# Kernel tuning notes

Hardware: AMD Instinct MI355X
Metric: run time of the kernel (lower is better)

The kernel has to match this reference:

```python
import jax, jax.numpy as jnp
import numpy as np


def _mlp(x, W1, b1, W2, b2, W3, b3):
    # flatten -> fc(784,512) -> relu -> fc(512,128) -> relu -> fc(128,C)
    h = x.reshape(x.shape[0], -1)
    h = jax.nn.relu(h @ W1.T + b1)
    h = jax.nn.relu(h @ W2.T + b2)
    return h @ W3.T + b3


def setup_inputs() -> dict:
    key = jax.random.key(0)
    ks = jax.random.split(key, 6)
    B, Bu, C, D = 65536, 4096, 10, 28 * 28
    return {
        "x": jax.random.uniform(ks[0], (B, 28, 28), jnp.float32),
        "y": jax.random.randint(ks[1], (B,), 0, C),
        "x_unlab": jax.random.uniform(ks[2], (Bu, 28, 28), jnp.float32),
        "W1": jax.random.normal(ks[3], (512, D), jnp.float32) * 0.03,
        "b1": jnp.zeros((512,), jnp.float32),
        "W2": jax.random.normal(ks[4], (128, 512), jnp.float32) * 0.05,
        "b2": jnp.zeros((128,), jnp.float32),
        "W3": jax.random.normal(ks[5], (C, 128), jnp.float32) * 0.08,
        "b3": jnp.zeros((C,), jnp.float32),
    }


def reference(x, y, x_unlab, W1, b1, W2, b2, W3, b3):
    n_classes = W3.shape[0]
    # ---- labeled branch: BCEWithLogitsLoss(mean) vs one-hot targets ----
    logits = _mlp(x, W1, b1, W2, b2, W3, b3)  # [B, C]
    t = jax.nn.one_hot(y, n_classes, dtype=logits.dtype)
    bce = jnp.mean(jnp.maximum(logits, 0.0) - logits * t
                   + jnp.log1p(jnp.exp(-jnp.abs(logits))))
    # ---- unlabeled branch: semantic loss ----
    # sem_loss(probs): s[c] = sum_i p_i[c] * prod_{j != i} (1 - p_j[c]);
    # return mean over classes of -log(s). Done in log domain with a single
    # O(Bu) leave-one-out sum instead of the original O(Bu^2) double loop.
    o_u = _mlp(x_unlab, W1, b1, W2, b2, W3, b3)       # [Bu, C]
    logp = jax.nn.log_sigmoid(o_u)                     # log p
    log1mp = jax.nn.log_sigmoid(-o_u)                  # log (1 - p)
    loo = jnp.sum(log1mp, axis=0, keepdims=True) - log1mp  # leave-one-out log-prod
    log_s = jax.scipy.special.logsumexp(logp + loo, axis=0)  # [C]
    sl = jnp.mean(-log_s)
    # compute_loss returns (bce, sl); stacked here as a length-2 vector
    return jnp.stack([bce, sl])
```

## Files before the change

### kernel.cpp

```cpp
#include <hip/hip_runtime.h>
#include <hip/hip_bf16.h>
#include <stdint.h>

typedef unsigned short ushort_t;
typedef __bf16 bf16x8 __attribute__((ext_vector_type(8)));
typedef float f32x4 __attribute__((ext_vector_type(4)));

__device__ __forceinline__ ushort_t f2bf(float f) {
    union { float f; unsigned u; } v; v.f = f;
    unsigned u = v.u;
    unsigned r = u + 0x7fffu + ((u >> 16) & 1u);
    return (ushort_t)(r >> 16);
}
__device__ __forceinline__ float bf2f(ushort_t h) {
    union { unsigned u; float f; } v; v.u = ((unsigned)h) << 16;
    return v.f;
}

#define GLDS16(gsrc, ldst)                                                    \
    __builtin_amdgcn_global_load_lds(                                         \
        (const __attribute__((address_space(1))) void*)(gsrc),                \
        (__attribute__((address_space(3))) void*)(ldst), 16, 0, 0)

__global__ __launch_bounds__(256) void prep_kernel(
    const float* __restrict__ W1, const float* __restrict__ W2,
    ushort_t* __restrict__ W1p, ushort_t* __restrict__ W2b,
    float* __restrict__ stats)
{
    int idx = blockIdx.x * 256 + threadIdx.x;
    if (idx < 512 * 800) {
        int n = idx / 800, k = idx - n * 800;
        W1p[idx] = (k < 784) ? f2bf(W1[n * 784 + k]) : (ushort_t)0;
    }
    if (idx < 128 * 512) W2b[idx] = f2bf(W2[idx]);
    if (idx == 0) stats[0] = 0.0f;
}

__global__ __launch_bounds__(256) void gemm1f_kernel(
    const float* __restrict__ x, const float* __restrict__ xu,
    const ushort_t* __restrict__ W1p, const float* __restrict__ b1,
    ushort_t* __restrict__ h1)
{
    __shared__ ushort_t As[2][128 * 32];
    __shared__ ushort_t Bs[2][128 * 32];

    const int b = blockIdx.x;
    const int xcd = b & 7, s = b >> 3;
    const int tile_n = s & 3;
    const int tile_m = xcd * 68 + (s >> 2);

    const int tid = threadIdx.x;
    const int w = tid >> 6, lane = tid & 63;
    const int wm = w >> 1, wn = w & 1;
    const int quad = lane >> 4, lc = lane & 15;
    const int row_in = lane >> 2;
    const int koff = (lane & 3) * 8;

    const int arow = tid >> 1;
    const int akoff = (tid & 1) * 16;
    const int grow = tile_m * 128 + arow;
    const float* asrc = (grow < 65536) ? (x + (size_t)grow * 784)
                                       : (xu + (size_t)(grow - 65536) * 784);
    ushort_t* adst0 = &As[0][arow * 32 + akoff];
    ushort_t* adst1 = &As[1][arow * 32 + akoff];

    f32x4 acc[4][4];
#pragma unroll
    for (int i = 0; i < 4; i++)
#pragma unroll
        for (int j = 0; j < 4; j++)
#pragma unroll
            for (int r = 0; r < 4; r++) acc[i][j][r] = 0.0f;

    float4 p0a, p0b, p0c, p0d, p1a, p1b, p1c, p1d;
    {
        const float4* q0 = (const float4*)(asrc + akoff);
        p0a = q0[0]; p0b = q0[1]; p0c = q0[2]; p0d = q0[3];
        const float4* q1 = (const float4*)(asrc + 32 + akoff);
        p1a = q1[0]; p1b = q1[1]; p1c = q1[2]; p1d = q1[3];
    }

    for (int k0 = 0; k0 < 800; k0 += 64) {
        const bool has2 = (k0 + 32) < 800;

#pragma unroll
        for (int c = 0; c < 2; c++) {
            int row = (w * 2 + c) * 16 + row_in;
            const ushort_t* srcB =
                W1p + (size_t)(tile_n * 128 + row) * 800 + k0 + koff;
            GLDS16(srcB, &Bs[0][(w * 2 + c) * 512]);
        }
        if (has2) {
#pragma unroll
            for (int c = 0; c < 2; c++) {
                int row = (w * 2 + c) * 16 + row_in;
                const ushort_t* srcB =
                    W1p + (size_t)(tile_n * 128 + row) * 800 + k0 + 32 + koff;
                GLDS16(srcB, &Bs[1][(w * 2 + c) * 512]);
            }
        }

        {
            uint4 lo, hi;
            if (k0 + akoff <= 768) {
                lo.x = ((unsigned)f2bf(p0a.y) << 16) | f2bf(p0a.x);
                lo.y = ((unsigned)f2bf(p0a.w) << 16) | f2bf(p0a.z);
                lo.z = ((unsigned)f2bf(p0b.y) << 16) | f2bf(p0b.x);
                lo.w = ((unsigned)f2bf(p0b.w) << 16) | f2bf(p0b.z);
                hi.x = ((unsigned)f2bf(p0c.y) << 16) | f2bf(p0c.x);
                hi.y = ((unsigned)f2bf(p0c.w) << 16) | f2bf(p0c.z);
                hi.z = ((unsigned)f2bf(p0d.y) << 16) | f2bf(p0d.x);
                hi.w = ((unsigned)f2bf(p0d.w) << 16) | f2bf(p0d.z);
            } else {
                lo = make_uint4(0, 0, 0, 0);
                hi = make_uint4(0, 0, 0, 0);
            }
            *(uint4*)adst0 = lo;
            *(uint4*)(adst0 + 8) = hi;
        }
        if (has2) {
            uint4 lo, hi;
            if (k0 + 32 + akoff <= 768) {
                lo.x = ((unsigned)f2bf(p1a.y) << 16) | f2bf(p1a.x);
                lo.y = ((unsigned)f2bf(p1a.w) << 16) | f2bf(p1a.z);
                lo.z = ((unsigned)f2bf(p1b.y) << 16) | f2bf(p1b.x);
                lo.w = ((unsigned)f2bf(p1b.w) << 16) | f2bf(p1b.z);
                hi.x = ((unsigned)f2bf(p1c.y) << 16) | f2bf(p1c.x);
                hi.y = ((unsigned)f2bf(p1c.w) << 16) | f2bf(p1c.z);
                hi.z = ((unsigned)f2bf(p1d.y) << 16) | f2bf(p1d.x);
                hi.w = ((unsigned)f2bf(p1d.w) << 16) | f2bf(p1d.z);
            } else {
                lo = make_uint4(0, 0, 0, 0);
                hi = make_uint4(0, 0, 0, 0);
            }
            *(uint4*)adst1 = lo;
            *(uint4*)(adst1 + 8) = hi;
        }

        {
            int kn0 = k0 + 64 + akoff;
            if (kn0 <= 768) {
                const float4* q = (const float4*)(asrc + kn0);
                p0a = q[0]; p0b = q[1]; p0c = q[2]; p0d = q[3];
            }
            int kn1 = k0 + 96 + akoff;
            if (kn1 <= 768) {
                const float4* q = (const float4*)(asrc + kn1);
                p1a = q[0]; p1b = q[1]; p1c = q[2]; p1d = q[3];
            }
        }
        __syncthreads();

        {
            bf16x8 af[4], bfr[4];
#pragma unroll
            for (int i = 0; i < 4; i++)
                af[i] = *(const bf16x8*)&As[0][(wm * 64 + i * 16 + lc) * 32 + quad * 8];
#pragma unroll
            for (int j = 0; j < 4; j++)
                bfr[j] = *(const bf16x8*)&Bs[0][(wn * 64 + j * 16 + lc) * 32 + quad * 8];
#pragma unroll
            for (int i = 0; i < 4; i++)
#pragma unroll
                for (int j = 0; j < 4; j++)
                    acc[i][j] = __builtin_amdgcn_mfma_f32_16x16x32_bf16(
                        af[i], bfr[j], acc[i][j], 0, 0, 0);
        }
        if (has2) {
            bf16x8 af[4], bfr[4];
#pragma unroll
            for (int i = 0; i < 4; i++)
                af[i] = *(const bf16x8*)&As[1][(wm * 64 + i * 16 + lc) * 32 + quad * 8];
#pragma unroll
            for (int j = 0; j < 4; j++)
                bfr[j] = *(const bf16x8*)&Bs[1][(wn * 64 + j * 16 + lc) * 32 + quad * 8];
#pragma unroll
            for (int i = 0; i < 4; i++)
#pragma unroll
                for (int j = 0; j < 4; j++)
                    acc[i][j] = __builtin_amdgcn_mfma_f32_16x16x32_bf16(
                        af[i], bfr[j], acc[i][j], 0, 0, 0);
        }
        __syncthreads();
    }

    float bias[4];
#pragma unroll
    for (int j = 0; j < 4; j++)
        bias[j] = b1[tile_n * 128 + wn * 64 + j * 16 + lc];
#pragma unroll
    for (int i = 0; i < 4; i++) {
        int gr0 = tile_m * 128 + wm * 64 + i * 16 + quad * 4;
#pragma unroll
        for (int j = 0; j < 4; j++) {
            int gc = tile_n * 128 + wn * 64 + j * 16 + lc;
#pragma unroll
            for (int r = 0; r < 4; r++) {
                float v = acc[i][j][r] + bias[j];
                v = fmaxf(v, 0.0f);
                h1[(size_t)(gr0 + r) * 512 + gc] = f2bf(v);
            }
        }
    }
}

__global__ __launch_bounds__(256) void gemm23_kernel(
    const ushort_t* __restrict__ h1, const ushort_t* __restrict__ W2b,
    const float* __restrict__ b2, const int* __restrict__ y,
    const float* __restrict__ W3, const float* __restrict__ b3,
    float* __restrict__ stats, float* __restrict__ logits_u)
{
    __shared__ ushort_t As[2][64 * 32];
    __shared__ ushort_t Bs[2][128 * 32];
    __shared__ float W3s[1280];
    __shared__ float b3s[10];
    __shared__ float red[4];

    const int tid = threadIdx.x;
    const int w = tid >> 6, lane = tid & 63;
    const int wm = w >> 1, wn = w & 1;
    const int quad = lane >> 4, lc = lane & 15;
    const int row_in = lane >> 2;
    const int koff = (lane & 3) * 8;
    const int tile_m = blockIdx.x;

    for (int i = tid; i < 1280; i += 256) W3s[i] = W3[i];
    if (tid < 10) b3s[tid] = b3[tid];

    f32x4 acc[2][4];
#pragma unroll
    for (int i = 0; i < 2; i++)
#pragma unroll
        for (int j = 0; j < 4; j++)
#pragma unroll
            for (int r = 0; r < 4; r++) acc[i][j][r] = 0.0f;

    for (int k0 = 0; k0 < 512; k0 += 64) {
#pragma unroll
        for (int p = 0; p < 2; p++) {
            {
                int rowA = w * 16 + row_in;
                const ushort_t* srcA =
                    h1 + (size_t)(tile_m * 64 + rowA) * 512 + k0 + p * 32 + koff;
                GLDS16(srcA, &As[p][w * 512]);
            }
#pragma unroll
            for (int c = 0; c < 2; c++) {
                int rowB = (w * 2 + c) * 16 + row_in;
                const ushort_t* srcB =
                    W2b + (size_t)rowB * 512 + k0 + p * 32 + koff;
                GLDS16(srcB, &Bs[p][(w * 2 + c) * 512]);
            }
        }
        __syncthreads();
#pragma unroll
        for (int p = 0; p < 2; p++) {
            bf16x8 af[2], bfr[4];
#pragma unroll
            for (int i = 0; i < 2; i++)
                af[i] = *(const bf16x8*)&As[p][(wm * 32 + i * 16 + lc) * 32 + quad * 8];
#pragma unroll
            for (int j = 0; j < 4; j++)
                bfr[j] = *(const bf16x8*)&Bs[p][(wn * 64 + j * 16 + lc) * 32 + quad * 8];
#pragma unroll
            for (int i = 0; i < 2; i++)
#pragma unroll
                for (int j = 0; j < 4; j++)
                    acc[i][j] = __builtin_amdgcn_mfma_f32_16x16x32_bf16(
                        af[i], bfr[j], acc[i][j], 0, 0, 0);
        }
        __syncthreads();
    }

    ushort_t* h2s = &Bs[0][0];
    float bias[4];
#pragma unroll
    for (int j = 0; j < 4; j++) bias[j] = b2[wn * 64 + j * 16 + lc];
#pragma unroll
    for (int i = 0; i < 2; i++) {
        int row0 = wm * 32 + i * 16 + quad * 4;
#pragma unroll
        for (int j = 0; j < 4; j++) {
            int col = wn * 64 + j * 16 + lc;
#pragma unroll
            for (int r = 0; r < 4; r++) {
                float v = fmaxf(acc[i][j][r] + bias[j], 0.0f);
                h2s[(row0 + r) * 128 + col] = f2bf(v);
            }
        }
    }
    __syncthreads();

    const size_t row0g = (size_t)tile_m * 64;
    float bce_part = 0.0f;
    for (int o = tid; o < 640; o += 256) {
        int r = o / 10, c = o - r * 10;
        size_t grw = row0g + r;
        float a = b3s[c];
        const ushort_t* hr = &h2s[r * 128];
        const float* wr = &W3s[c * 128];
#pragma unroll 8
        for (int k = 0; k < 128; k++) a += bf2f(hr[k]) * wr[k];
        if (grw < 65536) {
            float t = (y[grw] == c) ? 1.0f : 0.0f;
            bce_part += fmaxf(a, 0.0f) - a * t + log1pf(__expf(-fabsf(a)));
        } else {
            logits_u[(grw - 65536) * 10 + c] = a;
        }
    }
#pragma unroll
    for (int s = 32; s > 0; s >>= 1) bce_part += __shfl_down(bce_part, s, 64);
    if ((tid & 63) == 0) red[tid >> 6] = bce_part;
    __syncthreads();
    if (tid == 0) atomicAdd(stats, red[0] + red[1] + red[2] + red[3]);
}

__global__ __launch_bounds__(640) void finisher_kernel(
    const float* __restrict__ logits_u, const float* __restrict__ stats,
    float* __restrict__ out)
{
    __shared__ float Rs[64][10];
    __shared__ float Rm[64][10];
    __shared__ float Scol[10], Mcol[10];

    const int tid = threadIdx.x;
    const int g = tid / 10, c = tid - g * 10;
    float s = 0.0f, m = -1e30f;
    for (int i = g; i < 4096; i += 64) {
        float o = logits_u[i * 10 + c];
        s += fminf(-o, 0.0f) - log1pf(__expf(-fabsf(o)));
        m = fmaxf(m, o);
    }
    Rs[g][c] = s;
    Rm[g][c] = m;
    __syncthreads();
    if (tid < 10) {
        float ss = 0.0f, mm = -1e30f;
        for (int gg = 0; gg < 64; gg++) {
            ss += Rs[gg][tid];
            mm = fmaxf(mm, Rm[gg][tid]);
        }
        Scol[tid] = ss;
        Mcol[tid] = mm;
    }
    __syncthreads();
    float e = 0.0f;
    float mm = Mcol[c];
    for (int i = g; i < 4096; i += 64)
        e += __expf(logits_u[i * 10 + c] - mm);
    Rs[g][c] = e;
    __syncthreads();
    if (tid == 0) {
        float sl = 0.0f;
        for (int cc = 0; cc < 10; cc++) {
            float ee = 0.0f;
            for (int gg = 0; gg < 64; gg++) ee += Rs[gg][cc];
            sl += -(Scol[cc] + Mcol[cc] + __logf(ee));
        }
        sl *= 0.1f;
        out[0] = stats[0] * (1.0f / (65536.0f * 10.0f));
        out[1] = sl;
    }
}

extern "C" void kernel_launch(void* const* d_in, const int* in_sizes, int n_in,
                              void* d_out, int out_size, void* d_ws,
                              size_t ws_size, hipStream_t stream)
{
    const float* x  = (const float*)d_in[0];
    const int*   y  = (const int*)d_in[1];
    const float* xu = (const float*)d_in[2];
    const float* W1 = (const float*)d_in[3];
    const float* b1 = (const float*)d_in[4];
    const float* W2 = (const float*)d_in[5];
    const float* b2 = (const float*)d_in[6];
    const float* W3 = (const float*)d_in[7];
    const float* b3 = (const float*)d_in[8];
    float* out = (float*)d_out;

    char* ws = (char*)d_ws;
    ushort_t* W1p      = (ushort_t*)(ws + 0);
    ushort_t* W2b      = (ushort_t*)(ws + 819200);
    float*    stats    = (float*)(ws + 950272);
    float*    logits_u = (float*)(ws + 950528);
    ushort_t* h1       = (ushort_t*)(ws + 1114368);

    prep_kernel<<<1600, 256, 0, stream>>>(W1, W2, W1p, W2b, stats);
    gemm1f_kernel<<<2176, 256, 0, stream>>>(x, xu, W1p, b1, h1);
    gemm23_kernel<<<1088, 256, 0, stream>>>(h1, W2b, b2, y, W3, b3, stats,
                                            logits_u);
    finisher_kernel<<<1, 640, 0, stream>>>(logits_u, stats, out);
    (void)in_sizes; (void)n_in; (void)out_size; (void)ws_size;
}
```

Before: 503.3 us.

## Pre-convert inputs to bf16 and run LDS-free register-fed GEMM1

Adds a separate pass that converts x and x_unlab to a padded bf16 buffer in workspace, then a new GEMM1 kernel that loads MFMA operands straight from global memory into registers with software double-buffering, skipping LDS and __syncthreads. The goal is to remove in-loop fp32-to-bf16 conversion and LDS staging from the main GEMM. In exchange it adds an extra full read and write of the input (about 110 MB bf16 written, then re-read), and the direct global loads give no LDS reuse across waves. The new path only runs if the workspace is large enough, otherwise the old kernel is used.

Result: slower. 608.2 us (+20.8%).

```diff
diff --git a/kernel.cpp b/kernel.cpp
--- a/kernel.cpp
+++ b/kernel.cpp
@@ -34,6 +34,130 @@
     }
     if (idx < 128 * 512) W2b[idx] = f2bf(W2[idx]);
     if (idx == 0) stats[0] = 0.0f;
+}
+
+__global__ __launch_bounds__(256) void xconvert_kernel(
+    const float* __restrict__ x, const float* __restrict__ xu,
+    ushort_t* __restrict__ Xb)
+{
+    int idx = blockIdx.x * 256 + threadIdx.x;
+    int r = idx / 50, c = idx - r * 50;
+    uint4 lo, hi;
+    if (c < 49) {
+        const float* src = (r < 65536) ? (x + (size_t)r * 784)
+                                       : (xu + (size_t)(r - 65536) * 784);
+        const float4* p = (const float4*)(src + c * 16);
+        float4 f0 = p[0], f1 = p[1], f2 = p[2], f3 = p[3];
+        lo.x = ((unsigned)f2bf(f0.y) << 16) | f2bf(f0.x);
+        lo.y = ((unsigned)f2bf(f0.w) << 16) | f2bf(f0.z);
+        lo.z = ((unsigned)f2bf(f1.y) << 16) | f2bf(f1.x);
+        lo.w = ((unsigned)f2bf(f1.w) << 16) | f2bf(f1.z);
+        hi.x = ((unsigned)f2bf(f2.y) << 16) | f2bf(f2.x);
+        hi.y = ((unsigned)f2bf(f2.w) << 16) | f2bf(f2.z);
+        hi.z = ((unsigned)f2bf(f3.y) << 16) | f2bf(f3.x);
+        hi.w = ((unsigned)f2bf(f3.w) << 16) | f2bf(f3.z);
+    } else {
+        lo = make_uint4(0, 0, 0, 0);
+        hi = make_uint4(0, 0, 0, 0);
+    }
+    uint4* dst = (uint4*)(Xb + (size_t)r * 800 + c * 16);
+    dst[0] = lo;
+    dst[1] = hi;
+}
+
+__global__ __launch_bounds__(256) void gemm1reg_kernel(
+    const ushort_t* __restrict__ Xb, const ushort_t* __restrict__ W1p,
+    const float* __restrict__ b1, ushort_t* __restrict__ h1)
+{
+    const int b = blockIdx.x;
+    const int xcd = b & 7, s = b >> 3;
+    const int tile_n = s & 3;
+    const int tile_m = xcd * 68 + (s >> 2);
+
+    const int tid = threadIdx.x;
+    const int w = tid >> 6, lane = tid & 63;
+    const int wm = w >> 1, wn = w & 1;
+    const int quad = lane >> 4, lc = lane & 15;
+
+    const ushort_t* aptr[4];
+    const ushort_t* bptr[4];
+#pragma unroll
+    for (int i = 0; i < 4; i++) {
+        int row = tile_m * 128 + wm * 64 + i * 16 + lc;
+        aptr[i] = Xb + (size_t)row * 800 + quad * 8;
+    }
+#pragma unroll
+    for (int j = 0; j < 4; j++) {
+        int row = tile_n * 128 + wn * 64 + j * 16 + lc;
+        bptr[j] = W1p + (size_t)row * 800 + quad * 8;
+    }
+
+    f32x4 acc[4][4];
+#pragma unroll
+    for (int i = 0; i < 4; i++)
+#pragma unroll
+        for (int j = 0; j < 4; j++)
+#pragma unroll
+            for (int r = 0; r < 4; r++) acc[i][j][r] = 0.0f;
+
+    bf16x8 aA[4], bA[4], aB[4], bB[4];
+#pragma unroll
+    for (int i = 0; i < 4; i++) {
+        aA[i] = *(const bf16x8*)(aptr[i]);
+        bA[i] = *(const bf16x8*)(bptr[i]);
+    }
+
+    for (int k0 = 0; k0 < 800; k0 += 64) {
+        const bool hasB = (k0 + 32) < 800;
+        const bool hasN = (k0 + 64) < 800;
+        if (hasB) {
+#pragma unroll
+            for (int i = 0; i < 4; i++) {
+                aB[i] = *(const bf16x8*)(aptr[i] + k0 + 32);
+                bB[i] = *(const bf16x8*)(bptr[i] + k0 + 32);
+            }
+        }
+#pragma unroll
+        for (int i = 0; i < 4; i++)
+#pragma unroll
+            for (int j = 0; j < 4; j++)
+                acc[i][j] = __builtin_amdgcn_mfma_f32_16x16x32_bf16(
+                    aA[i], bA[j], acc[i][j], 0, 0, 0);
+        if (hasN) {
+#pragma unroll
+            for (int i = 0; i < 4; i++) {
+                aA[i] = *(const bf16x8*)(aptr[i] + k0 + 64);
+                bA[i] = *(const bf16x8*)(bptr[i] + k0 + 64);
+            }
+        }
+        if (hasB) {
+#pragma unroll
+            for (int i = 0; i < 4; i++)
+#pragma unroll
+                for (int j = 0; j < 4; j++)
+                    acc[i][j] = __builtin_amdgcn_mfma_f32_16x16x32_bf16(
+                        aB[i], bB[j], acc[i][j], 0, 0, 0);
+        }
+    }
+
+    float bias[4];
+#pragma unroll
+    for (int j = 0; j < 4; j++)
+        bias[j] = b1[tile_n * 128 + wn * 64 + j * 16 + lc];
+#pragma unroll
+    for (int i = 0; i < 4; i++) {
+        int gr0 = tile_m * 128 + wm * 64 + i * 16 + quad * 4;
+#pragma unroll
+        for (int j = 0; j < 4; j++) {
+            int gc = tile_n * 128 + wn * 64 + j * 16 + lc;
+#pragma unroll
+            for (int r = 0; r < 4; r++) {
+                float v = acc[i][j][r] + bias[j];
+                v = fmaxf(v, 0.0f);
+                h1[(size_t)(gr0 + r) * 512 + gc] = f2bf(v);
+            }
+        }
+    }
 }
 
 __global__ __launch_bounds__(256) void gemm1f_kernel(
@@ -82,7 +206,6 @@
 
     for (int k0 = 0; k0 < 800; k0 += 64) {
         const bool has2 = (k0 + 32) < 800;
-
 #pragma unroll
         for (int c = 0; c < 2; c++) {
             int row = (w * 2 + c) * 16 + row_in;
@@ -99,7 +222,6 @@
                 GLDS16(srcB, &Bs[1][(w * 2 + c) * 512]);
             }
         }
-
         {
             uint4 lo, hi;
             if (k0 + akoff <= 768) {
@@ -136,7 +258,6 @@
             *(uint4*)adst1 = lo;
             *(uint4*)(adst1 + 8) = hi;
         }
-
         {
             int kn0 = k0 + 64 + akoff;
             if (kn0 <= 768) {
@@ -150,7 +271,6 @@
             }
         }
         __syncthreads();
-
         {
             bf16x8 af[4], bfr[4];
 #pragma unroll
@@ -384,9 +504,16 @@
     float*    stats    = (float*)(ws + 950272);
     float*    logits_u = (float*)(ws + 950528);
     ushort_t* h1       = (ushort_t*)(ws + 1114368);
+    ushort_t* Xb       = (ushort_t*)(ws + 72417536);
+    const size_t FAST_WS_NEED = 183828736;
 
     prep_kernel<<<1600, 256, 0, stream>>>(W1, W2, W1p, W2b, stats);
-    gemm1f_kernel<<<2176, 256, 0, stream>>>(x, xu, W1p, b1, h1);
+    if (ws_size >= FAST_WS_NEED) {
+        xconvert_kernel<<<13600, 256, 0, stream>>>(x, xu, Xb);
+        gemm1reg_kernel<<<2176, 256, 0, stream>>>(Xb, W1p, b1, h1);
+    } else {
+        gemm1f_kernel<<<2176, 256, 0, stream>>>(x, xu, W1p, b1, h1);
+    }
     gemm23_kernel<<<1088, 256, 0, stream>>>(h1, W2b, b2, y, W3, b3, stats,
                                             logits_u);
     finisher_kernel<<<1, 640, 0, stream>>>(logits_u, stats, out);
```

## Fuse layer-1 and layer-2/3 GEMMs into one kernel keeping h1 in LDS

Applied to the files above, without the earlier changes.

Merges the first-layer GEMM and the second/third-layer kernel into a single kernel that processes 64-row tiles. Each tile loops over the four 128-column chunks of h1, stages each chunk in padded LDS, and accumulates it straight into the layer-2 result. This removes the global write and read of the large bf16 h1 intermediate and one kernel launch. In exchange, each block re-reads and re-converts its x rows four times and streams all of W1. The M tile also shrinks to 64 and W2 fragments are read directly from global memory, and the padded LDS stride adds a bank-conflict and alignment trade-off.

Result: slower. 576.3 us (+14.5%).

```diff
diff --git a/kernel.cpp b/kernel.cpp
--- a/kernel.cpp
+++ b/kernel.cpp
@@ -15,6 +15,9 @@
 __device__ __forceinline__ float bf2f(ushort_t h) {
     union { unsigned u; float f; } v; v.u = ((unsigned)h) << 16;
     return v.f;
+}
+__device__ __forceinline__ unsigned packbf(float a, float b) {
+    return ((unsigned)f2bf(b) << 16) | f2bf(a);
 }
 
 #define GLDS16(gsrc, ldst)                                                    \
@@ -36,18 +39,27 @@
     if (idx == 0) stats[0] = 0.0f;
 }
 
-__global__ __launch_bounds__(256) void gemm1f_kernel(
+#define AS_STRIDE 36
+#define H_STRIDE  136
+
+__global__ __launch_bounds__(256) void fused_kernel(
     const float* __restrict__ x, const float* __restrict__ xu,
-    const ushort_t* __restrict__ W1p, const float* __restrict__ b1,
-    ushort_t* __restrict__ h1)
+    const ushort_t* __restrict__ W1p, const ushort_t* __restrict__ W2b,
+    const float* __restrict__ b1, const float* __restrict__ b2,
+    const int* __restrict__ y, const float* __restrict__ W3,
+    const float* __restrict__ b3,
+    float* __restrict__ stats, float* __restrict__ logits_u)
 {
-    __shared__ ushort_t As[2][128 * 32];
-    __shared__ ushort_t Bs[2][128 * 32];
-
-    const int b = blockIdx.x;
-    const int xcd = b & 7, s = b >> 3;
-    const int tile_n = s & 3;
-    const int tile_m = xcd * 68 + (s >> 2);
+    __shared__ ushort_t smem[2 * 64 * AS_STRIDE + 2 * 128 * 32];
+    __shared__ float W3s[1280];
+    __shared__ float b3s[10];
+    __shared__ float red[4];
+
+    ushort_t* As0 = smem;
+    ushort_t* As1 = smem + 64 * AS_STRIDE;
+    ushort_t* Bs0 = smem + 2 * 64 * AS_STRIDE;
+    ushort_t* Bs1 = Bs0 + 128 * 32;
+    ushort_t* hs  = smem;
 
     const int tid = threadIdx.x;
     const int w = tid >> 6, lane = tid & 63;
@@ -55,249 +67,206 @@
     const int quad = lane >> 4, lc = lane & 15;
     const int row_in = lane >> 2;
     const int koff = (lane & 3) * 8;
-
-    const int arow = tid >> 1;
-    const int akoff = (tid & 1) * 16;
-    const int grow = tile_m * 128 + arow;
-    const float* asrc = (grow < 65536) ? (x + (size_t)grow * 784)
-                                       : (xu + (size_t)(grow - 65536) * 784);
-    ushort_t* adst0 = &As[0][arow * 32 + akoff];
-    ushort_t* adst1 = &As[1][arow * 32 + akoff];
-
-    f32x4 acc[4][4];
-#pragma unroll
-    for (int i = 0; i < 4; i++)
+    const int tile = blockIdx.x;
+    const size_t m0 = (size_t)tile * 64;
+
+    for (int i = tid; i < 1280; i += 256) W3s[i] = W3[i];
+    if (tid < 10) b3s[tid] = b3[tid];
+
+    const int arow = tid >> 2;
+    const int akoff = (tid & 3) * 8;
+    const size_t grow = m0 + arow;
+    const float* asrc = (grow < 65536) ? (x + grow * 784)
+                                       : (xu + (grow - 65536) * 784);
+    ushort_t* adst0 = &As0[arow * AS_STRIDE + akoff];
+    ushort_t* adst1 = &As1[arow * AS_STRIDE + akoff];
+
+    f32x4 h2acc[2][4];
+#pragma unroll
+    for (int i = 0; i < 2; i++)
 #pragma unroll
         for (int j = 0; j < 4; j++)
 #pragma unroll
-            for (int r = 0; r < 4; r++) acc[i][j][r] = 0.0f;
-
-    float4 p0a, p0b, p0c, p0d, p1a, p1b, p1c, p1d;
-    {
-        const float4* q0 = (const float4*)(asrc + akoff);
-        p0a = q0[0]; p0b = q0[1]; p0c = q0[2]; p0d = q0[3];
-        const float4* q1 = (const float4*)(asrc + 32 + akoff);
-        p1a = q1[0]; p1b = q1[1]; p1c = q1[2]; p1d = q1[3];
-    }
-
-    for (int k0 = 0; k0 < 800; k0 += 64) {
-        const bool has2 = (k0 + 32) < 800;
-
-#pragma unroll
-        for (int c = 0; c < 2; c++) {
-            int row = (w * 2 + c) * 16 + row_in;
-            const ushort_t* srcB =
-                W1p + (size_t)(tile_n * 128 + row) * 800 + k0 + koff;
-            GLDS16(srcB, &Bs[0][(w * 2 + c) * 512]);
-        }
-        if (has2) {
+            for (int r = 0; r < 4; r++) h2acc[i][j][r] = 0.0f;
+
+    for (int nc = 0; nc < 4; nc++) {
+        f32x4 acc[2][4];
+#pragma unroll
+        for (int i = 0; i < 2; i++)
+#pragma unroll
+            for (int j = 0; j < 4; j++)
+#pragma unroll
+                for (int r = 0; r < 4; r++) acc[i][j][r] = 0.0f;
+
+        float4 p0a, p0b, p1a, p1b;
+        {
+            const float4* q0 = (const float4*)(asrc + akoff);
+            p0a = q0[0]; p0b = q0[1];
+            const float4* q1 = (const float4*)(asrc + 32 + akoff);
+            p1a = q1[0]; p1b = q1[1];
+        }
+
+        for (int k0 = 0; k0 < 800; k0 += 64) {
+            const bool has2 = (k0 + 32) < 800;
 #pragma unroll
             for (int c = 0; c < 2; c++) {
                 int row = (w * 2 + c) * 16 + row_in;
                 const ushort_t* srcB =
-                    W1p + (size_t)(tile_n * 128 + row) * 800 + k0 + 32 + koff;
-                GLDS16(srcB, &Bs[1][(w * 2 + c) * 512]);
-            }
+                    W1p + (size_t)(nc * 128 + row) * 800 + k0 + koff;
+                GLDS16(srcB, &Bs0[(w * 2 + c) * 512]);
+            }
+            if (has2) {
+#pragma unroll
+                for (int c = 0; c < 2; c++) {
+                    int row = (w * 2 + c) * 16 + row_in;
+                    const ushort_t* srcB =
+                        W1p + (size_t)(nc * 128 + row) * 800 + k0 + 32 + koff;
+                    GLDS16(srcB, &Bs1[(w * 2 + c) * 512]);
+                }
+            }
+            {
+                uint4 u;
+                if (k0 + akoff <= 776) {
+                    u.x = packbf(p0a.x, p0a.y);
+                    u.y = packbf(p0a.z, p0a.w);
+                    u.z = packbf(p0b.x, p0b.y);
+                    u.w = packbf(p0b.z, p0b.w);
+                } else {
+                    u = make_uint4(0, 0, 0, 0);
+                }
+                *(uint4*)adst0 = u;
+            }
+            if (has2) {
+                uint4 u;
+                if (k0 + 32 + akoff <= 776) {
+                    u.x = packbf(p1a.x, p1a.y);
+                    u.y = packbf(p1a.z, p1a.w);
+                    u.z = packbf(p1b.x, p1b.y);
+                    u.w = packbf(p1b.z, p1b.w);
+                } else {
+                    u = make_uint4(0, 0, 0, 0);
+                }
+                *(uint4*)adst1 = u;
+            }
+            {
+                int kn0 = k0 + 64 + akoff;
+                if (kn0 <= 776) {
+                    const float4* q = (const float4*)(asrc + kn0);
+                    p0a = q[0]; p0b = q[1];
+                }
+                int kn1 = k0 + 96 + akoff;
+                if (kn1 <= 776) {
+                    const float4* q = (const float4*)(asrc + kn1);
+                    p1a = q[0]; p1b = q[1];
+                }
+            }
+            __syncthreads();
+            {
+                bf16x8 af[2], bfr[4];
+#pragma unroll
+                for (int i = 0; i < 2; i++)
+                    af[i] = *(const bf16x8*)
+                        &As0[(wm * 32 + i * 16 + lc) * AS_STRIDE + quad * 8];
+#pragma unroll
+                for (int j = 0; j < 4; j++)
+                    bfr[j] = *(const bf16x8*)
+                        &Bs0[(wn * 64 + j * 16 + lc) * 32 + quad * 8];
+#pragma unroll
+                for (int i = 0; i < 2; i++)
+#pragma unroll
+                    for (int j = 0; j < 4; j++)
+                        acc[i][j] = __builtin_amdgcn_mfma_f32_16x16x32_bf16(
+                            af[i], bfr[j], acc[i][j], 0, 0, 0);
+            }
+            if (has2) {
+                bf16x8 af[2], bfr[4];
+#pragma unroll
+                for (int i = 0; i < 2; i++)
+                    af[i] = *(const bf16x8*)
+                        &As1[(wm * 32 + i * 16 + lc) * AS_STRIDE + quad * 8];
+#pragma unroll
+                for (int j = 0; j < 4; j++)
+                    bfr[j] = *(const bf16x8*)
+                        &Bs1[(wn * 64 + j * 16 + lc) * 32 + quad * 8];
+#pragma unroll
+                for (int i = 0; i < 2; i++)
+#pragma unroll
+                    for (int j = 0; j < 4; j++)
+                        acc[i][j] = __builtin_amdgcn_mfma_f32_16x16x32_bf16(
+                            af[i], bfr[j], acc[i][j], 0, 0, 0);
+            }
+            __syncthreads();
         }
 
         {
-            uint4 lo, hi;
-            if (k0 + akoff <= 768) {
-                lo.x = ((unsigned)f2bf(p0a.y) << 16) | f2bf(p0a.x);
-                lo.y = ((unsigned)f2bf(p0a.w) << 16) | f2bf(p0a.z);
-                lo.z = ((unsigned)f2bf(p0b.y) << 16) | f2bf(p0b.x);
-                lo.w = ((unsigned)f2bf(p0b.w) << 16) | f2bf(p0b.z);
-                hi.x = ((unsigned)f2bf(p0c.y) << 16) | f2bf(p0c.x);
-                hi.y = ((unsigned)f2bf(p0c.w) << 16) | f2bf(p0c.z);
-                hi.z = ((unsigned)f2bf(p0d.y) << 16) | f2bf(p0d.x);
-                hi.w = ((unsigned)f2bf(p0d.w) << 16) | f2bf(p0d.z);
-            } else {
-                lo = make_uint4(0, 0, 0, 0);
-                hi = make_uint4(0, 0, 0, 0);
-            }
-            *(uint4*)adst0 = lo;
-            *(uint4*)(adst0 + 8) = hi;
-        }
-        if (has2) {
-            uint4 lo, hi;
-            if (k0 + 32 + akoff <= 768) {
-                lo.x = ((unsigned)f2bf(p1a.y) << 16) | f2bf(p1a.x);
-                lo.y = ((unsigned)f2bf(p1a.w) << 16) | f2bf(p1a.z);
-                lo.z = ((unsigned)f2bf(p1b.y) << 16) | f2bf(p1b.x);
-                lo.w = ((unsigned)f2bf(p1b.w) << 16) | f2bf(p1b.z);
-                hi.x = ((unsigned)f2bf(p1c.y) << 16) | f2bf(p1c.x);
-                hi.y = ((unsigned)f2bf(p1c.w) << 16) | f2bf(p1c.z);
-                hi.z = ((unsigned)f2bf(p1d.y) << 16) | f2bf(p1d.x);
-                hi.w = ((unsigned)f2bf(p1d.w) << 16) | f2bf(p1d.z);
-            } else {
-                lo = make_uint4(0, 0, 0, 0);
-                hi = make_uint4(0, 0, 0, 0);
-            }
-            *(uint4*)adst1 = lo;
-            *(uint4*)(adst1 + 8) = hi;
-        }
-
-        {
-            int kn0 = k0 + 64 + akoff;
-            if (kn0 <= 768) {
-                const float4* q = (const float4*)(asrc + kn0);
-                p0a = q[0]; p0b = q[1]; p0c = q[2]; p0d = q[3];
-            }
-            int kn1 = k0 + 96 + akoff;
-            if (kn1 <= 768) {
-                const float4* q = (const float4*)(asrc + kn1);
-                p1a = q[0]; p1b = q[1]; p1c = q[2]; p1d = q[3];
+            float bias[4];
+#pragma unroll
+            for (int j = 0; j < 4; j++)
+                bias[j] = b1[nc * 128 + wn * 64 + j * 16 + lc];
+#pragma unroll
+            for (int i = 0; i < 2; i++) {
+                int r0 = wm * 32 + i * 16 + quad * 4;
+#pragma unroll
+                for (int j = 0; j < 4; j++) {
+                    int col = wn * 64 + j * 16 + lc;
+#pragma unroll
+                    for (int r = 0; r < 4; r++) {
+                        float v = fmaxf(acc[i][j][r] + bias[j], 0.0f);
+                        hs[(r0 + r) * H_STRIDE + col] = f2bf(v);
+                    }
+                }
             }
         }
         __syncthreads();
 
-        {
-            bf16x8 af[4], bfr[4];
-#pragma unroll
-            for (int i = 0; i < 4; i++)
-                af[i] = *(const bf16x8*)&As[0][(wm * 64 + i * 16 + lc) * 32 + quad * 8];
+#pragma unroll
+        for (int p = 0; p < 4; p++) {
+            bf16x8 af[2], bfr[4];
+#pragma unroll
+            for (int i = 0; i < 2; i++)
+                af[i] = *(const bf16x8*)
+                    &hs[(wm * 32 + i * 16 + lc) * H_STRIDE + p * 32 + quad * 8];
 #pragma unroll
             for (int j = 0; j < 4; j++)
-                bfr[j] = *(const bf16x8*)&Bs[0][(wn * 64 + j * 16 + lc) * 32 + quad * 8];
-#pragma unroll
-            for (int i = 0; i < 4; i++)
+                bfr[j] = *(const bf16x8*)
+                    (W2b + (size_t)(wn * 64 + j * 16 + lc) * 512
+                         + nc * 128 + p * 32 + quad * 8);
+#pragma unroll
+            for (int i = 0; i < 2; i++)
 #pragma unroll
                 for (int j = 0; j < 4; j++)
-                    acc[i][j] = __builtin_amdgcn_mfma_f32_16x16x32_bf16(
-                        af[i], bfr[j], acc[i][j], 0, 0, 0);
-        }
-        if (has2) {
-            bf16x8 af[4], bfr[4];
-#pragma unroll
-            for (int i = 0; i < 4; i++)
-                af[i] = *(const bf16x8*)&As[1][(wm * 64 + i * 16 + lc) * 32 + quad * 8];
-#pragma unroll
-            for (int j = 0; j < 4; j++)
-                bfr[j] = *(const bf16x8*)&Bs[1][(wn * 64 + j * 16 + lc) * 32 + quad * 8];
-#pragma unroll
-            for (int i = 0; i < 4; i++)
-#pragma unroll
-                for (int j = 0; j < 4; j++)
-                    acc[i][j] = __builtin_amdgcn_mfma_f32_16x16x32_bf16(
-                        af[i], bfr[j], acc[i][j], 0, 0, 0);
+                    h2acc[i][j] = __builtin_amdgcn_mfma_f32_16x16x32_bf16(
+                        af[i], bfr[j], h2acc[i][j], 0, 0, 0);
         }
         __syncthreads();
     }
 
-    float bias[4];
-#pragma unroll
-    for (int j = 0; j < 4; j++)
-        bias[j] = b1[tile_n * 128 + wn * 64 + j * 16 + lc];
-#pragma unroll
-    for (int i = 0; i < 4; i++) {
-        int gr0 = tile_m * 128 + wm * 64 + i * 16 + quad * 4;
-#pragma unroll
-        for (int j = 0; j < 4; j++) {
-            int gc = tile_n * 128 + wn * 64 + j * 16 + lc;
-#pragma unroll
-            for (int r = 0; r < 4; r++) {
-                float v = acc[i][j][r] + bias[j];
-                v = fmaxf(v, 0.0f);
-                h1[(size_t)(gr0 + r) * 512 + gc] = f2bf(v);
-            }
-        }
-    }
-}
-
-__global__ __launch_bounds__(256) void gemm23_kernel(
-    const ushort_t* __restrict__ h1, const ushort_t* __restrict__ W2b,
-    const float* __restrict__ b2, const int* __restrict__ y,
-    const float* __restrict__ W3, const float* __restrict__ b3,
-    float* __restrict__ stats, float* __restrict__ logits_u)
-{
-    __shared__ ushort_t As[2][64 * 32];
-    __shared__ ushort_t Bs[2][128 * 32];
-    __shared__ float W3s[1280];
-    __shared__ float b3s[10];
-    __shared__ float red[4];
-
-    const int tid = threadIdx.x;
-    const int w = tid >> 6, lane = tid & 63;
-    const int wm = w >> 1, wn = w & 1;
-    const int quad = lane >> 4, lc = lane & 15;
-    const int row_in = lane >> 2;
-    const int koff = (lane & 3) * 8;
-    const int tile_m = blockIdx.x;
-
-    for (int i = tid; i < 1280; i += 256) W3s[i] = W3[i];
-    if (tid < 10) b3s[tid] = b3[tid];
-
-    f32x4 acc[2][4];
-#pragma unroll
-    for (int i = 0; i < 2; i++)
-#pragma unroll
-        for (int j = 0; j < 4; j++)
-#pragma unroll
-            for (int r = 0; r < 4; r++) acc[i][j][r] = 0.0f;
-
-    for (int k0 = 0; k0 < 512; k0 += 64) {
-#pragma unroll
-        for (int p = 0; p < 2; p++) {
-            {
-                int rowA = w * 16 + row_in;
-                const ushort_t* srcA =
-                    h1 + (size_t)(tile_m * 64 + rowA) * 512 + k0 + p * 32 + koff;
-                GLDS16(srcA, &As[p][w * 512]);
-            }
-#pragma unroll
-            for (int c = 0; c < 2; c++) {
-                int rowB = (w * 2 + c) * 16 + row_in;
-                const ushort_t* srcB =
-                    W2b + (size_t)rowB * 512 + k0 + p * 32 + koff;
-                GLDS16(srcB, &Bs[p][(w * 2 + c) * 512]);
-            }
-        }
-        __syncthreads();
-#pragma unroll
-        for (int p = 0; p < 2; p++) {
-            bf16x8 af[2], bfr[4];
-#pragma unroll
-            for (int i = 0; i < 2; i++)
-                af[i] = *(const bf16x8*)&As[p][(wm * 32 + i * 16 + lc) * 32 + quad * 8];
-#pragma unroll
-            for (int j = 0; j < 4; j++)
-                bfr[j] = *(const bf16x8*)&Bs[p][(wn * 64 + j * 16 + lc) * 32 + quad * 8];
-#pragma unroll
-            for (int i = 0; i < 2; i++)
-#pragma unroll
-                for (int j = 0; j < 4; j++)
-                    acc[i][j] = __builtin_amdgcn_mfma_f32_16x16x32_bf16(
-                        af[i], bfr[j], acc[i][j], 0, 0, 0);
-        }
-        __syncthreads();
-    }
-
-    ushort_t* h2s = &Bs[0][0];
-    float bias[4];
-#pragma unroll
-    for (int j = 0; j < 4; j++) bias[j] = b2[wn * 64 + j * 16 + lc];
-#pragma unroll
-    for (int i = 0; i < 2; i++) {
-        int row0 = wm * 32 + i * 16 + quad * 4;
-#pragma unroll
-        for (int j = 0; j < 4; j++) {
-            int col = wn * 64 + j * 16 + lc;
-#pragma unroll
-            for (int r = 0; r < 4; r++) {
-                float v = fmaxf(acc[i][j][r] + bias[j], 0.0f);
-                h2s[(row0 + r) * 128 + col] = f2bf(v);
-            }
-        }
-    }
-    __syncthreads();
-
-    const size_t row0g = (size_t)tile_m * 64;
+    {
+        float bias[4];
+#pragma unroll
+        for (int j = 0; j < 4; j++) bias[j] = b2[wn * 64 + j * 16 + lc];
+#pragma unroll
+        for (int i = 0; i < 2; i++) {
+            int r0 = wm * 32 + i * 16 + quad * 4;
+#pragma unroll
+            for (int j = 0; j < 4; j++) {
+                int col = wn * 64 + j * 16 + lc;
+#pragma unroll
+                for (int r = 0; r < 4; r++) {
+                    float v = fmaxf(h2acc[i][j][r] + bias[j], 0.0f);
+                    hs[(r0 + r) * H_STRIDE + col] = f2bf(v);
+                }
+            }
+        }
+    }
+    __syncthreads();
+
     float bce_part = 0.0f;
     for (int o = tid; o < 640; o += 256) {
         int r = o / 10, c = o - r * 10;
-        size_t grw = row0g + r;
+        size_t grw = m0 + r;
         float a = b3s[c];
-        const ushort_t* hr = &h2s[r * 128];
+        const ushort_t* hr = &hs[r * H_STRIDE];
         const float* wr = &W3s[c * 128];
 #pragma unroll 8
         for (int k = 0; k < 128; k++) a += bf2f(hr[k]) * wr[k];
@@ -383,12 +352,10 @@
     ushort_t* W2b      = (ushort_t*)(ws + 819200);
     float*    stats    = (float*)(ws + 950272);
     float*    logits_u = (float*)(ws + 950528);
-    ushort_t* h1       = (ushort_t*)(ws + 1114368);
 
     prep_kernel<<<1600, 256, 0, stream>>>(W1, W2, W1p, W2b, stats);
-    gemm1f_kernel<<<2176, 256, 0, stream>>>(x, xu, W1p, b1, h1);
-    gemm23_kernel<<<1088, 256, 0, stream>>>(h1, W2b, b2, y, W3, b3, stats,
-                                            logits_u);
+    fused_kernel<<<1088, 256, 0, stream>>>(x, xu, W1p, W2b, b1, b2, y, W3, b3,
+                                           stats, logits_u);
     finisher_kernel<<<1, 640, 0, stream>>>(logits_u, stats, out);
     (void)in_sizes; (void)n_in; (void)out_size; (void)ws_size;
 }
```
